# Kernel tuning notes

Measured on AMD Instinct MI355X. Metric: run time of the kernel, lower is better.

The kernel has to match this reference:

```python
import jax, jax.numpy as jnp
import numpy as np

# Dimensions: B batch, I genes per case, E embed dim, V sga vocab, NH heads,
# NB attention blocks, CAN cancer types, OUT output genes
B, I, E, V, NH, NB, CAN, OUT = 128, 800, 512, 19000, 8, 4, 10, 5000
MASK_VAL = -1e9


def setup_inputs() -> dict:
    key = jax.random.key(0)
    ks = jax.random.split(key, 10)
    s = 0.02
    sga = jax.random.randint(ks[0], (B, I), 0, V)            # 0 == padding
    can = jax.random.randint(ks[1], (B,), 0, CAN)
    emb_tables = jax.random.normal(ks[2], (NB, V + 1, E), jnp.float32) * s
    emb_tables = emb_tables.at[:, 0, :].set(0.0)              # padding_idx=0
    Wk = jax.random.normal(ks[3], (NB, E, E), jnp.float32) * s   # transform2Keys
    bk = jnp.zeros((NB, E), jnp.float32)
    Wq = jax.random.normal(ks[4], (NB, E, NH), jnp.float32) * s  # queryKeyMatch
    bq = jnp.zeros((NB, NH), jnp.float32)
    can_emb = jax.random.normal(ks[5], (CAN, E), jnp.float32) * s
    Wh = jax.random.normal(ks[6], (NB - 1, E, E), jnp.float32) * s  # residual linears (no bias)
    Wfinal = jax.random.normal(ks[7], (E, OUT), jnp.float32) * s    # final linear (no bias)
    return dict(sga=sga, can=can, emb_tables=emb_tables, Wk=Wk, bk=bk,
                Wq=Wq, bq=bq, can_emb=can_emb, Wh=Wh, Wfinal=Wfinal)


def _sga_block(sga, table, Wk_b, bk_b, Wq_b, bq_b):
    embs = table[sga]                                   # [B,I,E] gather
    keys = jnp.tanh(embs @ Wk_b + bk_b)                 # [B,I,E]
    scores = keys @ Wq_b + bq_b                         # [B,I,NH]
    scores = jnp.where(sga[..., None] == 0, MASK_VAL, scores)
    A = jax.nn.softmax(scores, axis=1)                  # softmax over genes I
    emb = jnp.einsum('bin,bie->be', A, embs)            # sum over heads + genes
    attn_wt = A.sum(axis=2)                             # [B,I]
    return emb, attn_wt


def reference(sga, can, emb_tables, Wk, bk, Wq, bq, can_emb, Wh, Wfinal):
    emb0, attn0 = _sga_block(sga, emb_tables[0], Wk[0], bk[0], Wq[0], bq[0])
    curr = jax.nn.relu(emb0 + can_emb[can])             # using_cancer_type=True
    attns = [attn0]
    hiddens = [curr]
    for i in range(1, NB):
        emb_i, attn_i = _sga_block(sga, emb_tables[i], Wk[i], bk[i], Wq[i], bq[i])
        curr = emb_i + curr @ Wh[i - 1]
        curr = jax.nn.relu(curr) if i < NB - 1 else jax.nn.sigmoid(curr)
        attns.append(attn_i)
        hiddens.append(curr)
    preds = curr @ Wfinal                               # [B,OUT]
    return preds, jnp.stack(attns), jnp.stack(hiddens)
```

## Files before the change

### kernel.cpp

```cpp
#include <hip/hip_runtime.h>
#include <hip/hip_bf16.h>

constexpr int Bn   = 128;
constexpr int In   = 800;
constexpr int En   = 512;
constexpr int V1   = 19001;
constexpr int NHn  = 8;
constexpr int NBn  = 4;
constexpr int OUTn = 5000;

constexpr int OFF_ATTN = Bn * OUTn;
constexpr int OFF_HID  = OFF_ATTN + NBn * Bn * In;

typedef __attribute__((ext_vector_type(8))) short bf16x8;
typedef __attribute__((ext_vector_type(8))) unsigned short u16x8;
typedef __attribute__((ext_vector_type(4))) float f32x4;

__device__ inline ushort f2bf(float x) {
    __hip_bfloat16 h = __float2bfloat16(x);
    return *reinterpret_cast<ushort*>(&h);
}
__device__ inline float bf2f(ushort u) {
    return __uint_as_float(((unsigned)u) << 16);
}
__device__ inline void gl_lds16(const ushort* g, ushort* l) {
    __builtin_amdgcn_global_load_lds(
        (const __attribute__((address_space(1))) void*)g,
        (__attribute__((address_space(3))) void*)l, 16, 0, 0);
}

__device__ inline float fast_tanh(float x) {
    const float e = __expf(2.0f * x);
    return 1.0f - 2.0f / (e + 1.0f);
}

#define DPP_XOR1(x) __int_as_float(__builtin_amdgcn_update_dpp( \
    0, __float_as_int(x), 0xB1, 0xF, 0xF, false))
#define DPP_XOR2(x) __int_as_float(__builtin_amdgcn_update_dpp( \
    0, __float_as_int(x), 0x4E, 0xF, 0xF, false))

__global__ __launch_bounds__(256)
void k_prep(const float* __restrict__ Wk, ushort* __restrict__ Wkt) {
    __shared__ float ts[64][65];
    const int n0 = blockIdx.x * 64, k0 = blockIdx.y * 64, nb = blockIdx.z;
    const int t = threadIdx.x;
    {
        const int kr = t >> 2, nc = (t & 3) * 16;
        const float* p = Wk + (((size_t)nb * En) + (k0 + kr)) * En + n0 + nc;
#pragma unroll
        for (int j = 0; j < 4; ++j) {
            const float4 v = *(const float4*)(p + j * 4);
            ts[kr][nc + j * 4 + 0] = v.x; ts[kr][nc + j * 4 + 1] = v.y;
            ts[kr][nc + j * 4 + 2] = v.z; ts[kr][nc + j * 4 + 3] = v.w;
        }
    }
    __syncthreads();
    {
        const int nr = t >> 2, kc = (t & 3) * 16;
        ushort* d = Wkt + (((size_t)nb * En) + (n0 + nr)) * En + k0 + kc;
        ushort4 o;
#pragma unroll
        for (int j = 0; j < 4; ++j) {
            o.x = f2bf(ts[kc + j * 4 + 0][nr]); o.y = f2bf(ts[kc + j * 4 + 1][nr]);
            o.z = f2bf(ts[kc + j * 4 + 2][nr]); o.w = f2bf(ts[kc + j * 4 + 3][nr]);
            *(ushort4*)(d + j * 4) = o;
        }
    }
}

template <bool TBF>
__global__ __launch_bounds__(256, 2)
void k_scores(const float* __restrict__ T, const ushort* __restrict__ Wkt,
              const float* __restrict__ bk, const float* __restrict__ Wq,
              float* __restrict__ scoresv, ushort* __restrict__ Tbf) {
    __shared__ ushort Bs[2][512][32];
    __shared__ union { ushort A[2][64][32]; float red[4][64][NHn]; } u;

    const int mblk = blockIdx.x, nb = blockIdx.y;
    const int v0 = mblk * 64;
    const int tid = threadIdx.x, lane = tid & 63, w = tid >> 6;
    const int q = lane >> 4, c = lane & 15;
    const int gsw = (q ^ (c & 3)) * 8;

    const float*  Tb = T + (size_t)nb * V1 * En;
    const ushort* Wn = Wkt + (size_t)nb * En * En;

    const int arow = tid >> 2, akq = tid & 3;
    const int aswz = (akq ^ (arow & 3)) * 8;
    const int vra = v0 + arow;
    const float* agp = Tb + (size_t)vra * En + akq * 8;
    ushort* tsp = Tbf + ((size_t)nb * V1 + vra) * En + akq * 8;

    f32x4 acc[4][8];
#pragma unroll
    for (int mt = 0; mt < 4; ++mt)
#pragma unroll
        for (int nt = 0; nt < 8; ++nt) acc[mt][nt] = (f32x4)0.0f;

    auto stageB = [&](int buf, int k0) {
#pragma unroll
        for (int j = 0; j < 8; ++j) {
            const int nrow = (w * 8 + j) * 16;
            const int r = nrow + (lane >> 2);
            const int gf = (lane & 3) ^ ((lane >> 2) & 3);
            const ushort* gp = Wn + (size_t)r * En + k0 + gf * 8;
            gl_lds16(gp, &Bs[buf][nrow][0]);
        }
    };
    auto loadA = [&](int k0, float4& f0, float4& f1) {
        if (vra < V1) {
            f0 = *(const float4*)(agp + k0);
            f1 = *(const float4*)(agp + k0 + 4);
        } else {
            f0 = make_float4(0.f, 0.f, 0.f, 0.f);
            f1 = f0;
        }
    };
    u16x8 stash;
    auto writeA = [&](int buf, int k0, float4 f0, float4 f1) {
        u16x8 o;
        o[0] = f2bf(f0.x); o[1] = f2bf(f0.y); o[2] = f2bf(f0.z); o[3] = f2bf(f0.w);
        o[4] = f2bf(f1.x); o[5] = f2bf(f1.y); o[6] = f2bf(f1.z); o[7] = f2bf(f1.w);
        *(u16x8*)&u.A[buf][arow][aswz] = o;
        if (TBF && vra < V1) {
            const int itIdx = k0 >> 5;
            if ((itIdx & 1) == 0) {
                stash = o;
            } else {
                *(u16x8*)(tsp + k0 - 32) = stash;
                *(u16x8*)(tsp + k0)      = o;
            }
        }
    };

    stageB(0, 0);
    {
        float4 f0, f1;
        loadA(0, f0, f1);
        writeA(0, 0, f0, f1);
    }
    __syncthreads();

    for (int it = 0; it < 16; ++it) {
        const int cur = it & 1, nxt = cur ^ 1;
        const int k0n = (it + 1) * 32;
        float4 p0, p1;
        if (it < 15) {
            stageB(nxt, k0n);
            loadA(k0n, p0, p1);
        }
        bf16x8 aF[4], bF[8];
#pragma unroll
        for (int mt = 0; mt < 4; ++mt)
            aF[mt] = *(bf16x8*)&u.A[cur][mt * 16 + c][gsw];
#pragma unroll
        for (int nt = 0; nt < 8; ++nt)
            bF[nt] = *(bf16x8*)&Bs[cur][w * 128 + nt * 16 + c][gsw];
#pragma unroll
        for (int nt = 0; nt < 8; ++nt)
#pragma unroll
            for (int mt = 0; mt < 4; ++mt)
                acc[mt][nt] = __builtin_amdgcn_mfma_f32_16x16x32_bf16(
                    aF[mt], bF[nt], acc[mt][nt], 0, 0, 0);
        if (it < 15) writeA(nxt, k0n, p0, p1);
        __syncthreads();
    }

#pragma unroll
    for (int nt = 0; nt < 8; ++nt) {
        const int col = w * 128 + nt * 16 + c;
        const float bkv = bk[nb * En + col];
#pragma unroll
        for (int mt = 0; mt < 4; ++mt)
#pragma unroll
            for (int r = 0; r < 4; ++r)
                acc[mt][nt][r] = fast_tanh(acc[mt][nt][r] + bkv);
    }

    for (int h = 0; h < NHn; ++h) {
        float wqh[8];
#pragma unroll
        for (int nt = 0; nt < 8; ++nt) {
            const int col = w * 128 + nt * 16 + c;
            wqh[nt] = Wq[((size_t)nb * En + col) * NHn + h];
        }
        float p[4][4];
#pragma unroll
        for (int mt = 0; mt < 4; ++mt)
#pragma unroll
            for (int r = 0; r < 4; ++r) {
                float s = 0.f;
#pragma unroll
                for (int nt = 0; nt < 8; ++nt) s += acc[mt][nt][r] * wqh[nt];
                s += DPP_XOR1(s);
                s += DPP_XOR2(s);
                s += __shfl_xor(s, 4, 64);
                s += __shfl_xor(s, 8, 64);
                p[mt][r] = s;
            }
        if (c == h) {
#pragma unroll
            for (int mt = 0; mt < 4; ++mt)
#pragma unroll
                for (int r = 0; r < 4; ++r)
                    u.red[w][mt * 16 + q * 4 + r][h] = p[mt][r];
        }
    }
    __syncthreads();

    for (int idx = tid; idx < 64 * NHn; idx += 256) {
        const int row = idx >> 3, h = idx & 7;
        const int vr = v0 + row;
        if (vr < V1)
            scoresv[((size_t)nb * V1 + vr) * NHn + h] =
                u.red[0][row][h] + u.red[1][row][h] +
                u.red[2][row][h] + u.red[3][row][h];
    }
}

__global__ __launch_bounds__(256)
void k_softmax(const int* __restrict__ sga, const float* __restrict__ scoresv,
               float* __restrict__ attn_out) {
    const int b  = blockIdx.x;
    const int nb = blockIdx.y;
    const int tid = threadIdx.x;
    const int lane = tid & 63;
    const int wid  = tid >> 6;
    __shared__ float red[4 * NHn];

    float sc[4][NHn];
    int ivals[4];
#pragma unroll
    for (int s = 0; s < 4; ++s) {
        const int i = tid + s * 256;
        ivals[s] = i;
        if (i < In) {
            const int v = sga[b * In + i];
            const float4 s0 = *(const float4*)(scoresv + ((size_t)nb * V1 + v) * NHn);
            const float4 s1 = *(const float4*)(scoresv + ((size_t)nb * V1 + v) * NHn + 4);
            sc[s][0] = s0.x; sc[s][1] = s0.y; sc[s][2] = s0.z; sc[s][3] = s0.w;
            sc[s][4] = s1.x; sc[s][5] = s1.y; sc[s][6] = s1.z; sc[s][7] = s1.w;
            if (v == 0) {
#pragma unroll
                for (int n = 0; n < NHn; ++n) sc[s][n] = -1e9f;
            }
        } else {
#pragma unroll
            for (int n = 0; n < NHn; ++n) sc[s][n] = -3.0e38f;
        }
    }

    float lm[NHn];
#pragma unroll
    for (int n = 0; n < NHn; ++n)
        lm[n] = fmaxf(fmaxf(sc[0][n], sc[1][n]), fmaxf(sc[2][n], sc[3][n]));
#pragma unroll
    for (int m = 1; m < 64; m <<= 1) {
#pragma unroll
        for (int n = 0; n < NHn; ++n) lm[n] = fmaxf(lm[n], __shfl_xor(lm[n], m, 64));
    }
    if (lane == 0) {
#pragma unroll
        for (int n = 0; n < NHn; ++n) red[wid * NHn + n] = lm[n];
    }
    __syncthreads();
    float M[NHn];
#pragma unroll
    for (int n = 0; n < NHn; ++n)
        M[n] = fmaxf(fmaxf(red[n], red[NHn + n]), fmaxf(red[2 * NHn + n], red[3 * NHn + n]));
    __syncthreads();

    float ls[NHn];
#pragma unroll
    for (int n = 0; n < NHn; ++n) ls[n] = 0.f;
#pragma unroll
    for (int s = 0; s < 4; ++s) {
#pragma unroll
        for (int n = 0; n < NHn; ++n) {
            sc[s][n] = expf(sc[s][n] - M[n]);
            ls[n] += sc[s][n];
        }
    }
#pragma unroll
    for (int m = 1; m < 64; m <<= 1) {
#pragma unroll
        for (int n = 0; n < NHn; ++n) ls[n] += __shfl_xor(ls[n], m, 64);
    }
    if (lane == 0) {
#pragma unroll
        for (int n = 0; n < NHn; ++n) red[wid * NHn + n] = ls[n];
    }
    __syncthreads();
    float inv[NHn];
#pragma unroll
    for (int n = 0; n < NHn; ++n) {
        const float S = red[n] + red[NHn + n] + red[2 * NHn + n] + red[3 * NHn + n];
        inv[n] = 1.0f / S;
    }

#pragma unroll
    for (int s = 0; s < 4; ++s) {
        if (ivals[s] < In) {
            float w = 0.f;
#pragma unroll
            for (int n = 0; n < NHn; ++n) w += sc[s][n] * inv[n];
            attn_out[((size_t)nb * Bn + b) * In + ivals[s]] = w;
        }
    }
}

template <bool TBF>
__global__ __launch_bounds__(512)
void k_emb(const int* __restrict__ sga, const float* __restrict__ attn,
           const float* __restrict__ T, const ushort* __restrict__ Tbf,
           float* __restrict__ emb) {
    const int b  = blockIdx.x;
    const int nb = blockIdx.y;
    __shared__ int   sv[In];
    __shared__ float sw[In];
    __shared__ float pa[8][En];
    for (int idx = threadIdx.x; idx < In; idx += 512) {
        sv[idx] = sga[b * In + idx];
        sw[idx] = attn[((size_t)nb * Bn + b) * In + idx];
    }
    __syncthreads();
    const int wave = threadIdx.x >> 6, lane = threadIdx.x & 63;
    float a[8];
#pragma unroll
    for (int j = 0; j < 8; ++j) a[j] = 0.f;

    if (TBF) {
        const ushort* Tb = Tbf + (size_t)nb * V1 * En;
#pragma unroll 10
        for (int g = 0; g < 100; ++g) {
            const int i = wave * 100 + g;
            const int v = sv[i];
            const float w = sw[i];
            const u16x8 t = *(const u16x8*)(Tb + (size_t)v * En + lane * 8);
#pragma unroll
            for (int j = 0; j < 8; ++j) a[j] += w * bf2f(t[j]);
        }
    } else {
        const float* Tb = T + (size_t)nb * V1 * En;
#pragma unroll 10
        for (int g = 0; g < 100; ++g) {
            const int i = wave * 100 + g;
            const int v = sv[i];
            const float w = sw[i];
            const float4* p = (const float4*)(Tb + (size_t)v * En) + lane * 2;
            const float4 t0 = p[0], t1 = p[1];
            a[0] += w * t0.x; a[1] += w * t0.y; a[2] += w * t0.z; a[3] += w * t0.w;
            a[4] += w * t1.x; a[5] += w * t1.y; a[6] += w * t1.z; a[7] += w * t1.w;
        }
    }
#pragma unroll
    for (int j = 0; j < 8; ++j) pa[wave][lane * 8 + j] = a[j];
    __syncthreads();
    const int t = threadIdx.x;
    float s = 0.f;
#pragma unroll
    for (int wv = 0; wv < 8; ++wv) s += pa[wv][t];
    emb[((size_t)nb * Bn + b) * En + t] = s;
}

__global__ __launch_bounds__(256)
void k_step0(const float* __restrict__ emb0, const int* __restrict__ can,
             const float* __restrict__ can_emb, float* __restrict__ cur,
             float* __restrict__ hid) {
    const int b = blockIdx.x;
    const int e0 = threadIdx.x * 2;
    const int c = can[b];
    float2 v = *(const float2*)(emb0 + (size_t)b * En + e0);
    const float2 ce = *(const float2*)(can_emb + (size_t)c * En + e0);
    v.x = fmaxf(v.x + ce.x, 0.f);
    v.y = fmaxf(v.y + ce.y, 0.f);
    *(float2*)(cur + (size_t)b * En + e0) = v;
    *(float2*)(hid + (size_t)b * En + e0) = v;
}

__global__ __launch_bounds__(256)
void k_step(const float* __restrict__ embi, const float* __restrict__ prev,
            const float* __restrict__ Whi, float* __restrict__ cur,
            float* __restrict__ hid, const int sig) {
    const int b = blockIdx.x, cc = blockIdx.y;
    __shared__ float pr[En];
    __shared__ float part[2][128];
    pr[threadIdx.x]       = prev[(size_t)b * En + threadIdx.x];
    pr[threadIdx.x + 256] = prev[(size_t)b * En + threadIdx.x + 256];
    __syncthreads();
    const int col = cc * 128 + (threadIdx.x & 127);
    const int kh  = threadIdx.x >> 7;
    float s = 0.f;
    const float* Wp = Whi + (size_t)(kh * 256) * En + col;
#pragma unroll 8
    for (int k = 0; k < 256; ++k) s += pr[kh * 256 + k] * Wp[(size_t)k * En];
    part[kh][threadIdx.x & 127] = s;
    __syncthreads();
    if (threadIdx.x < 128) {
        float a = part[0][threadIdx.x] + part[1][threadIdx.x] +
                  embi[(size_t)b * En + col];
        if (sig) a = 1.0f / (1.0f + expf(-a));
        else     a = fmaxf(a, 0.f);
        cur[(size_t)b * En + col] = a;
        hid[(size_t)b * En + col] = a;
    }
}

__global__ __launch_bounds__(256, 2)
void k_preds(const float* __restrict__ cur, const float* __restrict__ Wf,
             float* __restrict__ preds) {
    __shared__ float cs[32 * En];
    const int nt = blockIdx.x;
    const int bt = blockIdx.y;
    for (int idx = threadIdx.x; idx < 32 * 128; idx += 256) {
        const int row = idx >> 7;
        const int c4  = (idx & 127) << 2;
        *(float4*)(cs + row * En + c4) =
            *(const float4*)(cur + (size_t)(bt * 32 + row) * En + c4);
    }
    __syncthreads();
    const int lane = threadIdx.x & 63;
    const int rgrp = threadIdx.x >> 6;
    const int col = nt * 64 + lane;
    float acc[8];
#pragma unroll
    for (int j = 0; j < 8; ++j) acc[j] = 0.f;
    const bool ok = (col < OUTn);
    for (int k = 0; k < En; k += 4) {
        float w0 = 0.f, w1 = 0.f, w2 = 0.f, w3 = 0.f;
        if (ok) {
            w0 = Wf[(size_t)(k + 0) * OUTn + col];
            w1 = Wf[(size_t)(k + 1) * OUTn + col];
            w2 = Wf[(size_t)(k + 2) * OUTn + col];
            w3 = Wf[(size_t)(k + 3) * OUTn + col];
        }
#pragma unroll
        for (int j = 0; j < 8; ++j) {
            const float4 cv = *(const float4*)(cs + (rgrp * 8 + j) * En + k);
            acc[j] += cv.x * w0 + cv.y * w1 + cv.z * w2 + cv.w * w3;
        }
    }
    if (ok) {
#pragma unroll
        for (int j = 0; j < 8; ++j)
            preds[(size_t)(bt * 32 + rgrp * 8 + j) * OUTn + col] = acc[j];
    }
}

extern "C" void kernel_launch(void* const* d_in, const int* in_sizes, int n_in,
                              void* d_out, int out_size, void* d_ws, size_t ws_size,
                              hipStream_t stream) {
    const int*   sga     = (const int*)d_in[0];
    const int*   can     = (const int*)d_in[1];
    const float* T       = (const float*)d_in[2];
    const float* Wk      = (const float*)d_in[3];
    const float* bk      = (const float*)d_in[4];
    const float* Wq      = (const float*)d_in[5];
    const float* can_emb = (const float*)d_in[7];
    const float* Wh      = (const float*)d_in[8];
    const float* Wf      = (const float*)d_in[9];

    float* out = (float*)d_out;
    float* ws  = (float*)d_ws;

    float* scoresv = ws;
    float* embw    = scoresv + (size_t)NBn * V1 * NHn;
    float* cur0    = embw + (size_t)NBn * Bn * En;
    float* cur1    = cur0 + (size_t)Bn * En;
    ushort* Wkt    = (ushort*)(cur1 + (size_t)Bn * En);
    ushort* Tbf    = Wkt + (size_t)NBn * En * En;
    const size_t need_full =
        (size_t)(scoresv - ws) * 4 +
        ((size_t)NBn * V1 * NHn + (size_t)NBn * Bn * En + 2 * (size_t)Bn * En) * 4 +
        (size_t)NBn * En * En * 2 + (size_t)NBn * V1 * En * 2;
    const bool useTbf = (ws_size >= need_full);

    float* preds_out = out;
    float* attn_out  = out + OFF_ATTN;
    float* hid_out   = out + OFF_HID;

    k_prep<<<dim3(8, 8, NBn), 256, 0, stream>>>(Wk, Wkt);
    if (useTbf)
        k_scores<true><<<dim3((V1 + 63) / 64, NBn), 256, 0, stream>>>(
            T, Wkt, bk, Wq, scoresv, Tbf);
    else
        k_scores<false><<<dim3((V1 + 63) / 64, NBn), 256, 0, stream>>>(
            T, Wkt, bk, Wq, scoresv, Tbf);
    k_softmax<<<dim3(Bn, NBn), 256, 0, stream>>>(sga, scoresv, attn_out);
    if (useTbf)
        k_emb<true><<<dim3(Bn, NBn), 512, 0, stream>>>(sga, attn_out, T, Tbf, embw);
    else
        k_emb<false><<<dim3(Bn, NBn), 512, 0, stream>>>(sga, attn_out, T, Tbf, embw);
    k_step0<<<Bn, 256, 0, stream>>>(embw, can, can_emb, cur0, hid_out);
    k_step<<<dim3(Bn, 4), 256, 0, stream>>>(embw + 1 * Bn * En, cur0,
                                            Wh + 0 * En * En, cur1,
                                            hid_out + 1 * (size_t)Bn * En, 0);
    k_step<<<dim3(Bn, 4), 256, 0, stream>>>(embw + 2 * Bn * En, cur1,
                                            Wh + 1 * En * En, cur0,
                                            hid_out + 2 * (size_t)Bn * En, 0);
    k_step<<<dim3(Bn, 4), 256, 0, stream>>>(embw + 3 * Bn * En, cur0,
                                            Wh + 2 * En * En, cur1,
                                            hid_out + 3 * (size_t)Bn * En, 1);
    k_preds<<<dim3((OUTn + 63) / 64, Bn / 32), 256, 0, stream>>>(cur1, Wf, preds_out);
}
```

Measured before the change: 544.9 us.

## Split fp32-to-bf16 table conversion into separate kernel and load A via async LDS

Adds a standalone grid-stride kernel that converts the full embedding tables to bf16. The scores GEMM then streams bf16 A tiles directly into LDS with the same global-to-LDS async copy used for B, instead of loading fp32, converting in registers and writing the bf16 copy as a side effect. This removes per-thread conversion and register staging from the MFMA loop and halves A read traffic inside the GEMM. In exchange it adds an extra full pass over the fp32 tables plus the bf16 write, and one more kernel launch.

```diff
diff --git a/kernel.cpp b/kernel.cpp
--- a/kernel.cpp
+++ b/kernel.cpp
@@ -68,11 +68,25 @@
     }
 }
 
-template <bool TBF>
+__global__ __launch_bounds__(256)
+void k_cvt(const float* __restrict__ T, ushort* __restrict__ Tbf,
+           const long long n8) {
+    const long long stride = (long long)gridDim.x * 256;
+    for (long long i = (long long)blockIdx.x * 256 + threadIdx.x; i < n8;
+         i += stride) {
+        const float4 f0 = *(const float4*)(T + i * 8);
+        const float4 f1 = *(const float4*)(T + i * 8 + 4);
+        u16x8 o;
+        o[0] = f2bf(f0.x); o[1] = f2bf(f0.y); o[2] = f2bf(f0.z); o[3] = f2bf(f0.w);
+        o[4] = f2bf(f1.x); o[5] = f2bf(f1.y); o[6] = f2bf(f1.z); o[7] = f2bf(f1.w);
+        *(u16x8*)(Tbf + i * 8) = o;
+    }
+}
+
 __global__ __launch_bounds__(256, 2)
-void k_scores(const float* __restrict__ T, const ushort* __restrict__ Wkt,
-              const float* __restrict__ bk, const float* __restrict__ Wq,
-              float* __restrict__ scoresv, ushort* __restrict__ Tbf) {
+void k_scores_fast(const ushort* __restrict__ Tbf, const ushort* __restrict__ Wkt,
+                   const float* __restrict__ bk, const float* __restrict__ Wq,
+                   float* __restrict__ scoresv) {
     __shared__ ushort Bs[2][512][32];
     __shared__ union { ushort A[2][64][32]; float red[4][64][NHn]; } u;
 
@@ -82,6 +96,126 @@
     const int q = lane >> 4, c = lane & 15;
     const int gsw = (q ^ (c & 3)) * 8;
 
+    const ushort* Ab = Tbf + (size_t)nb * V1 * En;
+    const ushort* Wn = Wkt + (size_t)nb * En * En;
+
+    const int ar  = w * 16 + (lane >> 2);
+    const int ag  = (lane & 3) ^ ((lane >> 2) & 3);
+    const int vrow = min(v0 + ar, V1 - 1);
+    const ushort* agp = Ab + (size_t)vrow * En + ag * 8;
+
+    f32x4 acc[4][8];
+#pragma unroll
+    for (int mt = 0; mt < 4; ++mt)
+#pragma unroll
+        for (int nt = 0; nt < 8; ++nt) acc[mt][nt] = (f32x4)0.0f;
+
+    auto stageB = [&](int buf, int k0) {
+#pragma unroll
+        for (int j = 0; j < 8; ++j) {
+            const int nrow = (w * 8 + j) * 16;
+            const int r = nrow + (lane >> 2);
+            const int gf = (lane & 3) ^ ((lane >> 2) & 3);
+            const ushort* gp = Wn + (size_t)r * En + k0 + gf * 8;
+            gl_lds16(gp, &Bs[buf][nrow][0]);
+        }
+    };
+    auto stageA = [&](int buf, int k0) {
+        gl_lds16(agp + k0, &u.A[buf][w * 16][0]);
+    };
+
+    stageA(0, 0);
+    stageB(0, 0);
+    __syncthreads();
+
+    for (int it = 0; it < 16; ++it) {
+        const int cur = it & 1, nxt = cur ^ 1;
+        if (it < 15) {
+            const int k0n = (it + 1) * 32;
+            stageA(nxt, k0n);
+            stageB(nxt, k0n);
+        }
+        bf16x8 aF[4], bF[8];
+#pragma unroll
+        for (int mt = 0; mt < 4; ++mt)
+            aF[mt] = *(bf16x8*)&u.A[cur][mt * 16 + c][gsw];
+#pragma unroll
+        for (int nt = 0; nt < 8; ++nt)
+            bF[nt] = *(bf16x8*)&Bs[cur][w * 128 + nt * 16 + c][gsw];
+#pragma unroll
+        for (int nt = 0; nt < 8; ++nt)
+#pragma unroll
+            for (int mt = 0; mt < 4; ++mt)
+                acc[mt][nt] = __builtin_amdgcn_mfma_f32_16x16x32_bf16(
+                    aF[mt], bF[nt], acc[mt][nt], 0, 0, 0);
+        __syncthreads();
+    }
+
+#pragma unroll
+    for (int nt = 0; nt < 8; ++nt) {
+        const int col = w * 128 + nt * 16 + c;
+        const float bkv = bk[nb * En + col];
+#pragma unroll
+        for (int mt = 0; mt < 4; ++mt)
+#pragma unroll
+            for (int r = 0; r < 4; ++r)
+                acc[mt][nt][r] = fast_tanh(acc[mt][nt][r] + bkv);
+    }
+
+    for (int h = 0; h < NHn; ++h) {
+        float wqh[8];
+#pragma unroll
+        for (int nt = 0; nt < 8; ++nt) {
+            const int col = w * 128 + nt * 16 + c;
+            wqh[nt] = Wq[((size_t)nb * En + col) * NHn + h];
+        }
+        float p[4][4];
+#pragma unroll
+        for (int mt = 0; mt < 4; ++mt)
+#pragma unroll
+            for (int r = 0; r < 4; ++r) {
+                float s = 0.f;
+#pragma unroll
+                for (int nt = 0; nt < 8; ++nt) s += acc[mt][nt][r] * wqh[nt];
+                s += DPP_XOR1(s);
+                s += DPP_XOR2(s);
+                s += __shfl_xor(s, 4, 64);
+                s += __shfl_xor(s, 8, 64);
+                p[mt][r] = s;
+            }
+        if (c == h) {
+#pragma unroll
+            for (int mt = 0; mt < 4; ++mt)
+#pragma unroll
+                for (int r = 0; r < 4; ++r)
+                    u.red[w][mt * 16 + q * 4 + r][h] = p[mt][r];
+        }
+    }
+    __syncthreads();
+
+    for (int idx = tid; idx < 64 * NHn; idx += 256) {
+        const int row = idx >> 3, h = idx & 7;
+        const int vr = v0 + row;
+        if (vr < V1)
+            scoresv[((size_t)nb * V1 + vr) * NHn + h] =
+                u.red[0][row][h] + u.red[1][row][h] +
+                u.red[2][row][h] + u.red[3][row][h];
+    }
+}
+
+__global__ __launch_bounds__(256, 2)
+void k_scores_slow(const float* __restrict__ T, const ushort* __restrict__ Wkt,
+                   const float* __restrict__ bk, const float* __restrict__ Wq,
+                   float* __restrict__ scoresv) {
+    __shared__ ushort Bs[2][512][32];
+    __shared__ union { ushort A[2][64][32]; float red[4][64][NHn]; } u;
+
+    const int mblk = blockIdx.x, nb = blockIdx.y;
+    const int v0 = mblk * 64;
+    const int tid = threadIdx.x, lane = tid & 63, w = tid >> 6;
+    const int q = lane >> 4, c = lane & 15;
+    const int gsw = (q ^ (c & 3)) * 8;
+
     const float*  Tb = T + (size_t)nb * V1 * En;
     const ushort* Wn = Wkt + (size_t)nb * En * En;
 
@@ -89,7 +223,6 @@
     const int aswz = (akq ^ (arow & 3)) * 8;
     const int vra = v0 + arow;
     const float* agp = Tb + (size_t)vra * En + akq * 8;
-    ushort* tsp = Tbf + ((size_t)nb * V1 + vra) * En + akq * 8;
 
     f32x4 acc[4][8];
 #pragma unroll
@@ -116,28 +249,18 @@
             f1 = f0;
         }
     };
-    u16x8 stash;
-    auto writeA = [&](int buf, int k0, float4 f0, float4 f1) {
+    auto writeA = [&](int buf, float4 f0, float4 f1) {
         u16x8 o;
         o[0] = f2bf(f0.x); o[1] = f2bf(f0.y); o[2] = f2bf(f0.z); o[3] = f2bf(f0.w);
         o[4] = f2bf(f1.x); o[5] = f2bf(f1.y); o[6] = f2bf(f1.z); o[7] = f2bf(f1.w);
         *(u16x8*)&u.A[buf][arow][aswz] = o;
-        if (TBF && vra < V1) {
-            const int itIdx = k0 >> 5;
-            if ((itIdx & 1) == 0) {
-                stash = o;
-            } else {
-                *(u16x8*)(tsp + k0 - 32) = stash;
-                *(u16x8*)(tsp + k0)      = o;
-            }
-        }
     };
 
     stageB(0, 0);
     {
         float4 f0, f1;
         loadA(0, f0, f1);
-        writeA(0, 0, f0, f1);
+        writeA(0, f0, f1);
     }
     __syncthreads();
 
@@ -162,7 +285,7 @@
             for (int mt = 0; mt < 4; ++mt)
                 acc[mt][nt] = __builtin_amdgcn_mfma_f32_16x16x32_bf16(
                     aF[mt], bF[nt], acc[mt][nt], 0, 0, 0);
-        if (it < 15) writeA(nxt, k0n, p0, p1);
+        if (it < 15) writeA(nxt, p0, p1);
         __syncthreads();
     }
 
@@ -480,12 +603,15 @@
     float* hid_out   = out + OFF_HID;
 
     k_prep<<<dim3(8, 8, NBn), 256, 0, stream>>>(Wk, Wkt);
-    if (useTbf)
-        k_scores<true><<<dim3((V1 + 63) / 64, NBn), 256, 0, stream>>>(
-            T, Wkt, bk, Wq, scoresv, Tbf);
-    else
-        k_scores<false><<<dim3((V1 + 63) / 64, NBn), 256, 0, stream>>>(
-            T, Wkt, bk, Wq, scoresv, Tbf);
+    if (useTbf) {
+        const long long n8 = (long long)NBn * V1 * En / 8;
+        k_cvt<<<2048, 256, 0, stream>>>(T, Tbf, n8);
+        k_scores_fast<<<dim3((V1 + 63) / 64, NBn), 256, 0, stream>>>(
+            Tbf, Wkt, bk, Wq, scoresv);
+    } else {
+        k_scores_slow<<<dim3((V1 + 63) / 64, NBn), 256, 0, stream>>>(
+            T, Wkt, bk, Wq, scoresv);
+    }
     k_softmax<<<dim3(Bn, NBn), 256, 0, stream>>>(sga, scoresv, attn_out);
     if (useTbf)
         k_emb<true><<<dim3(Bn, NBn), 512, 0, stream>>>(sga, attn_out, T, Tbf, embw);
```

Result: no change. 541.7 us (-0.6%).
